# Performance work log

Hardware: AMD Instinct MI355X
Metric: run time of the kernel (lower is better)

## Reference

```python
import jax, jax.numpy as jnp
import numpy as np

B, S, D, H, L = 32, 1024, 512, 8, 4
DH = D // H
FF = D            # dim_feedforward == hidden_dim in the original ctor call
LOC_D, TD_D = 16, 8
TD_EMB = 3        # time_dist_embed_dim
POI = 21          # poi vocab
POI_EMB = 3
ADDR_IN = 1 + POI_EMB
FC = 32           # fc_hidden_dim
NEG = -1e9


def setup_inputs() -> dict:
    key = jax.random.key(0)
    ks = jax.random.split(key, 20)
    g = lambda i, shape, s=0.02: jax.random.normal(ks[i], shape, jnp.float32) * s
    return {
        "addr": jax.random.normal(ks[0], (B, 1), jnp.float32),
        "loc_dense_seq": jax.random.normal(ks[1], (B, S, LOC_D), jnp.float32),
        "time_dist_seq": jax.random.normal(ks[2], (B, S, TD_D), jnp.float32),
        "Wtd": g(3, (TD_D, TD_EMB)), "btd": jnp.zeros((TD_EMB,), jnp.float32),
        "Wemb": g(4, (LOC_D + TD_EMB, D)), "bemb": jnp.zeros((D,), jnp.float32),
        "Wqkv": g(5, (L, D, 3 * D)), "bqkv": jnp.zeros((L, 3 * D), jnp.float32),
        "Wo": g(6, (L, D, D)), "bo": jnp.zeros((L, D), jnp.float32),
        "ln1_g": jnp.ones((L, D), jnp.float32), "ln1_b": jnp.zeros((L, D), jnp.float32),
        "W1": g(7, (L, D, FF)), "b1": jnp.zeros((L, FF), jnp.float32),
        "W2": g(8, (L, FF, D)), "b2": jnp.zeros((L, D), jnp.float32),
        "ln2_g": jnp.ones((L, D), jnp.float32), "ln2_b": jnp.zeros((L, D), jnp.float32),
        "poi_emb": g(9, (POI, POI_EMB), 1.0),
        "Wa": g(10, (ADDR_IN, FC)), "ba": jnp.zeros((FC,), jnp.float32),
        "Wout": g(11, (D, FC)),
        "Wcomb": g(12, (FC, 1)),
        "addr_type": jax.random.randint(ks[13], (B, 1), 0, POI),
        "data_length": jax.random.randint(ks[14], (B,), 1, S + 1),
    }


def _ln(x, g, b, eps=1e-5):
    m = x.mean(-1, keepdims=True)
    v = ((x - m) ** 2).mean(-1, keepdims=True)
    return (x - m) / jnp.sqrt(v + eps) * g + b


def reference(addr, loc_dense_seq, time_dist_seq, Wtd, btd, Wemb, bemb, Wqkv,
              bqkv, Wo, bo, ln1_g, ln1_b, W1, b1, W2, b2, ln2_g, ln2_b,
              poi_emb, Wa, ba, Wout, Wcomb, addr_type, data_length):
    valid = jnp.arange(S)[None, :] < data_length[:, None]            # [B,S]
    td = time_dist_seq @ Wtd + btd                                   # [B,S,3]
    x = jnp.concatenate([loc_dense_seq, td], axis=-1) @ Wemb + bemb  # [B,S,D]
    scale = 1.0 / jnp.sqrt(jnp.float32(DH))
    for l in range(L):  # post-norm TransformerEncoderLayer (relu, eval/no-dropout)
        qkv = x @ Wqkv[l] + bqkv[l]
        q, k, v = jnp.split(qkv, 3, axis=-1)
        q = q.reshape(B, S, H, DH)
        k = k.reshape(B, S, H, DH)
        v = v.reshape(B, S, H, DH)
        scores = jnp.einsum('bqhd,bkhd->bhqk', q, k) * scale
        scores = jnp.where(valid[:, None, None, :], scores, NEG)     # mask padded keys
        attn = jax.nn.softmax(scores, axis=-1)
        ctx = jnp.einsum('bhqk,bkhd->bqhd', attn, v).reshape(B, S, D)
        x = _ln(x + ctx @ Wo[l] + bo[l], ln1_g[l], ln1_b[l])
        ff = jax.nn.relu(x @ W1[l] + b1[l]) @ W2[l] + b2[l]
        x = _ln(x + ff, ln2_g[l], ln2_b[l])
    # per-sample addr branch (vectorized over the original python loop)
    addr_inp = jnp.concatenate([addr, poi_emb[addr_type[:, 0]]], axis=-1)  # [B,4]
    a = addr_inp @ Wa + ba                                                 # [B,FC]
    o = (jnp.tanh(x @ Wout + a[:, None, :]) @ Wcomb)[..., 0]              # [B,S]
    logits = jnp.where(valid, o, NEG)
    logp = jax.nn.log_softmax(logits, axis=1)  # log_softmax over valid positions only
    return jnp.where(valid, logp, 0.0)
```

## Files before the change

### kernel.cpp

```cpp
#include <hip/hip_runtime.h>
#include <stdint.h>


typedef unsigned short u16;
typedef __attribute__((ext_vector_type(8))) short short8;
typedef __attribute__((ext_vector_type(4))) float f32x4;

constexpr int Bn = 32, Sn = 1024, Dn = 512, Hn = 8, Ln = 4;
constexpr int BS = Bn * Sn;

__device__ __forceinline__ float b2f(u16 u) {
    union { uint32_t i; float f; } v; v.i = ((uint32_t)u) << 16; return v.f;
}
__device__ __forceinline__ u16 f2b(float f) {
    union { float f; uint32_t i; } v; v.f = f;
    uint32_t r = v.i + 0x7fffu + ((v.i >> 16) & 1u);
    return (u16)(r >> 16);
}
__device__ __forceinline__ float getf(const void* p, size_t i, int F) {
    return F ? ((const float*)p)[i] : b2f(((const u16*)p)[i]);
}

__device__ __forceinline__ void cp16(void* lds, const void* g) {
    __builtin_amdgcn_global_load_lds(
        (__attribute__((address_space(1))) void*)(uintptr_t)g,
        (__attribute__((address_space(3))) void*)(uint32_t)(uintptr_t)lds,
        16, 0, 0);
}

__global__ __launch_bounds__(256)
void detect_kernel(const void* loc, int* flag)
{
    __shared__ int cnt;
    if (threadIdx.x == 0) cnt = 0;
    __syncthreads();
    const u16* p = (const u16*)loc;
    int c = 0;
    for (int i = threadIdx.x; i < 2048; i += 256) {
        const float v = b2f(p[i]);
        if (!(fabsf(v) <= 100.0f)) c++;
    }
    atomicAdd(&cnt, c);
    __syncthreads();
    if (threadIdx.x == 0) *flag = (cnt >= 64) ? 1 : 0;
}

__global__ __launch_bounds__(256)
void gemm_bt(const u16* __restrict__ A, const u16* __restrict__ Bt,
             const void* __restrict__ bias, int boff, u16* __restrict__ C,
             int N, int K, int relu, const int* __restrict__ flagp)
{
    __shared__ __align__(16) u16 As[128 * 32];
    __shared__ __align__(16) u16 Bs[128 * 32];
    const int F = *flagp;
    const int tid = threadIdx.x;
    const int lane = tid & 63, w = tid >> 6;
    const int wm = w >> 1, wn = w & 1;
    const int quad = lane >> 4, l16 = lane & 15;
    const int bn0 = blockIdx.x * 128, bm0 = blockIdx.y * 128;

    const f32x4 vzero = {0.f, 0.f, 0.f, 0.f};
    f32x4 acc[4][4];
#pragma unroll
    for (int i = 0; i < 4; i++)
#pragma unroll
        for (int j = 0; j < 4; j++) acc[i][j] = vzero;

    const int i0 = tid, i1 = tid + 256;
    const u16* a0 = A + (size_t)(bm0 + (i0 >> 2)) * K + (i0 & 3) * 8;
    const u16* a1 = A + (size_t)(bm0 + (i1 >> 2)) * K + (i1 & 3) * 8;
    const u16* b0 = Bt + (size_t)(bn0 + (i0 >> 2)) * K + (i0 & 3) * 8;
    const u16* b1 = Bt + (size_t)(bn0 + (i1 >> 2)) * K + (i1 & 3) * 8;

    for (int k0 = 0; k0 < K; k0 += 32) {
        cp16(As + i0 * 8, a0 + k0);
        cp16(As + i1 * 8, a1 + k0);
        cp16(Bs + i0 * 8, b0 + k0);
        cp16(Bs + i1 * 8, b1 + k0);
        __syncthreads();
        short8 af[4], bfr[4];
#pragma unroll
        for (int t = 0; t < 4; t++)
            af[t] = *(const short8*)&As[(wm * 64 + t * 16 + l16) * 32 + quad * 8];
#pragma unroll
        for (int t = 0; t < 4; t++)
            bfr[t] = *(const short8*)&Bs[(wn * 64 + t * 16 + l16) * 32 + quad * 8];
#pragma unroll
        for (int tm = 0; tm < 4; tm++)
#pragma unroll
            for (int tn = 0; tn < 4; tn++)
                acc[tm][tn] = __builtin_amdgcn_mfma_f32_16x16x32_bf16(
                    af[tm], bfr[tn], acc[tm][tn], 0, 0, 0);
        __syncthreads();
    }
#pragma unroll
    for (int tm = 0; tm < 4; tm++)
#pragma unroll
        for (int tn = 0; tn < 4; tn++) {
            const int col = bn0 + wn * 64 + tn * 16 + l16;
            const float bv = getf(bias, (size_t)boff + col, F);
#pragma unroll
            for (int r = 0; r < 4; r++) {
                const int row = bm0 + wm * 64 + tm * 16 + quad * 4 + r;
                float v = acc[tm][tn][r] + bv;
                if (relu) v = fmaxf(v, 0.0f);
                C[(size_t)row * N + col] = f2b(v);
            }
        }
}

__global__ __launch_bounds__(256)
void attn_kernel(const u16* __restrict__ qkv, const int* __restrict__ dlen,
                 u16* __restrict__ ctx)
{
    const int qt = blockIdx.x, h = blockIdx.y, b = blockIdx.z;
    const int tid = threadIdx.x, lane = tid & 63, w = tid >> 6;
    const int quad = lane >> 4, l16 = lane & 15;
    const int len = dlen[b];
    __shared__ __align__(16) u16 Vt[64 * 72];
    __shared__ __align__(16) u16 Pl[4][16 * 64];
    const size_t rs = 3 * Dn;
    const u16* base = qkv + (size_t)b * Sn * rs;
    const int q0 = qt * 64 + w * 16;

    short8 qf[2];
#pragma unroll
    for (int s = 0; s < 2; s++)
        qf[s] = *(const short8*)(base + (size_t)(q0 + l16) * rs + h * 64 + quad * 8 + 32 * s);

    const f32x4 vzero = {0.f, 0.f, 0.f, 0.f};
    f32x4 O[4];
#pragma unroll
    for (int t = 0; t < 4; t++) O[t] = vzero;
    float m_i[4] = {-1e9f, -1e9f, -1e9f, -1e9f};
    float l_i[4] = {0.f, 0.f, 0.f, 0.f};

    const int nkt = (len + 63) >> 6;
    for (int kt = 0; kt < nkt; kt++) {
        const int k0 = kt * 64;
        {
            const int key = tid >> 2, f0 = (tid & 3) * 16;
            const u16* vp = base + (size_t)(k0 + key) * rs + 2 * Dn + h * 64 + f0;
            short8 v0 = *(const short8*)vp;
            short8 v1 = *(const short8*)(vp + 8);
#pragma unroll
            for (int j = 0; j < 8; j++) {
                Vt[(f0 + j) * 72 + key]     = (u16)v0[j];
                Vt[(f0 + 8 + j) * 72 + key] = (u16)v1[j];
            }
        }
        __syncthreads();

        f32x4 sacc[4];
#pragma unroll
        for (int tn = 0; tn < 4; tn++) {
            const int key = k0 + tn * 16 + l16;
            const u16* kp = base + (size_t)key * rs + Dn + h * 64 + quad * 8;
            short8 kf0 = *(const short8*)kp;
            short8 kf1 = *(const short8*)(kp + 32);
            f32x4 z = vzero;
            z = __builtin_amdgcn_mfma_f32_16x16x32_bf16(qf[0], kf0, z, 0, 0, 0);
            sacc[tn] = __builtin_amdgcn_mfma_f32_16x16x32_bf16(qf[1], kf1, z, 0, 0, 0);
        }
        float sv[4][4], mt[4] = {-1e9f, -1e9f, -1e9f, -1e9f};
#pragma unroll
        for (int tn = 0; tn < 4; tn++) {
            const bool ok = (k0 + tn * 16 + l16) < len;
#pragma unroll
            for (int r = 0; r < 4; r++) {
                const float v = ok ? sacc[tn][r] * 0.125f : -1e9f;
                sv[tn][r] = v;
                mt[r] = fmaxf(mt[r], v);
            }
        }
#pragma unroll
        for (int r = 0; r < 4; r++)
#pragma unroll
            for (int o = 1; o < 16; o <<= 1)
                mt[r] = fmaxf(mt[r], __shfl_xor(mt[r], o, 64));
        float alpha[4];
#pragma unroll
        for (int r = 0; r < 4; r++) {
            const float mn = fmaxf(m_i[r], mt[r]);
            alpha[r] = __expf(m_i[r] - mn);
            m_i[r] = mn;
        }
        float rsum[4] = {0.f, 0.f, 0.f, 0.f};
#pragma unroll
        for (int tn = 0; tn < 4; tn++)
#pragma unroll
            for (int r = 0; r < 4; r++) {
                const float p = __expf(sv[tn][r] - m_i[r]);
                rsum[r] += p;
                Pl[w][(quad * 4 + r) * 64 + tn * 16 + l16] = f2b(p);
            }
#pragma unroll
        for (int r = 0; r < 4; r++) {
#pragma unroll
            for (int o = 1; o < 16; o <<= 1)
                rsum[r] += __shfl_xor(rsum[r], o, 64);
            l_i[r] = l_i[r] * alpha[r] + rsum[r];
        }
#pragma unroll
        for (int t = 0; t < 4; t++)
#pragma unroll
            for (int r = 0; r < 4; r++)
                O[t][r] *= alpha[r];
#pragma unroll
        for (int s = 0; s < 2; s++) {
            short8 pf = *(const short8*)&Pl[w][l16 * 64 + quad * 8 + 32 * s];
#pragma unroll
            for (int t = 0; t < 4; t++) {
                short8 vf = *(const short8*)&Vt[(t * 16 + l16) * 72 + quad * 8 + 32 * s];
                O[t] = __builtin_amdgcn_mfma_f32_16x16x32_bf16(pf, vf, O[t], 0, 0, 0);
            }
        }
        __syncthreads();
    }
#pragma unroll
    for (int t = 0; t < 4; t++)
#pragma unroll
        for (int r = 0; r < 4; r++) {
            const int q = q0 + quad * 4 + r;
            ctx[(size_t)(b * Sn + q) * Dn + h * 64 + t * 16 + l16] = f2b(O[t][r] / l_i[r]);
        }
}

__global__ __launch_bounds__(256)
void ln_res(u16* __restrict__ x, const u16* __restrict__ t,
            const void* __restrict__ g, const void* __restrict__ bta, int off,
            const int* __restrict__ flagp)
{
    const int F = *flagp;
    const int w = threadIdx.x >> 6, lane = threadIdx.x & 63;
    const size_t row = (size_t)blockIdx.x * 4 + w;
    u16* xp = x + row * Dn;
    const u16* tp = t + row * Dn;
    float v[8]; float s = 0.f;
#pragma unroll
    for (int i = 0; i < 8; i++) {
        const int c = lane + i * 64;
        v[i] = b2f(xp[c]) + b2f(tp[c]);
        s += v[i];
    }
#pragma unroll
    for (int o = 1; o < 64; o <<= 1) s += __shfl_xor(s, o, 64);
    const float mean = s * (1.0f / 512.0f);
    float q = 0.f;
#pragma unroll
    for (int i = 0; i < 8; i++) { const float d = v[i] - mean; q += d * d; }
#pragma unroll
    for (int o = 1; o < 64; o <<= 1) q += __shfl_xor(q, o, 64);
    const float inv = rsqrtf(q * (1.0f / 512.0f) + 1e-5f);
#pragma unroll
    for (int i = 0; i < 8; i++) {
        const int c = lane + i * 64;
        xp[c] = f2b((v[i] - mean) * inv * getf(g, off + c, F) + getf(bta, off + c, F));
    }
}

__global__ __launch_bounds__(256)
void embed_kernel(const void* __restrict__ loc, const void* __restrict__ tds,
                  const void* __restrict__ Wtd, const void* __restrict__ btd,
                  const void* __restrict__ Wemb, const void* __restrict__ bemb,
                  u16* __restrict__ x, const int* __restrict__ flagp)
{
    const int F = *flagp;
    const int token = blockIdx.x;
    const int tid = threadIdx.x;
    __shared__ float inv[19];
    if (tid < 16) {
        inv[tid] = getf(loc, (size_t)token * 16 + tid, F);
    } else if (tid < 19) {
        const int e = tid - 16;
        float a = getf(btd, e, F);
        for (int j = 0; j < 8; j++)
            a += getf(tds, (size_t)token * 8 + j, F) * getf(Wtd, j * 3 + e, F);
        inv[tid] = a;
    }
    __syncthreads();
    for (int d = tid; d < Dn; d += 256) {
        float a = getf(bemb, d, F);
#pragma unroll
        for (int i = 0; i < 19; i++) a += inv[i] * getf(Wemb, (size_t)i * Dn + d, F);
        x[(size_t)token * Dn + d] = f2b(a);
    }
}

__global__ __launch_bounds__(256)
void transpose_w(const void* __restrict__ src, u16* __restrict__ dst,
                 int K, int N, const int* __restrict__ flagp)
{
    const int F = *flagp;
    __shared__ u16 tile[32][33];
    const size_t ls = (size_t)K * N;
    const size_t sb = (size_t)blockIdx.z * ls;
    u16* d = dst + blockIdx.z * ls;
    const int tx = threadIdx.x & 31, ty = threadIdx.x >> 5;
    const int n0 = blockIdx.x * 32, k0 = blockIdx.y * 32;
#pragma unroll
    for (int i = 0; i < 32; i += 8)
        tile[ty + i][tx] = f2b(getf(src, sb + (size_t)(k0 + ty + i) * N + n0 + tx, F));
    __syncthreads();
#pragma unroll
    for (int i = 0; i < 32; i += 8)
        d[(size_t)(n0 + ty + i) * K + k0 + tx] = tile[tx][ty + i];
}

__global__ __launch_bounds__(256)
void final_proj(const u16* __restrict__ x, const void* __restrict__ Wout,
                const void* __restrict__ Wcomb, const void* __restrict__ addr,
                const void* __restrict__ poi, const int* __restrict__ atype,
                const void* __restrict__ Wa, const void* __restrict__ ba,
                float* __restrict__ logits, const int* __restrict__ flagp)
{
    const int F = *flagp;
    __shared__ float xs[8][512];
    const int tid = threadIdx.x;
    const int t0 = blockIdx.x * 8;
    for (int i = tid; i < 8 * 512; i += 256) {
        const int tk = i >> 9, d = i & 511;
        xs[tk][d] = b2f(x[(size_t)(t0 + tk) * Dn + d]);
    }
    __syncthreads();
    const int half = tid >> 5, j = tid & 31;
    const int token = t0 + half;
    const int b = token >> 10;
    const int ty = atype[b];
    float a = getf(ba, j, F) + getf(addr, b, F) * getf(Wa, j, F);
#pragma unroll
    for (int e = 0; e < 3; e++)
        a += getf(poi, ty * 3 + e, F) * getf(Wa, (1 + e) * 32 + j, F);
    float s = a;
    for (int k = 0; k < 512; k++) s += xs[half][k] * getf(Wout, (size_t)k * 32 + j, F);
    float o = tanhf(s) * getf(Wcomb, j, F);
#pragma unroll
    for (int off = 1; off < 32; off <<= 1) o += __shfl_xor(o, off, 64);
    if (j == 0) logits[token] = o;
}

__global__ __launch_bounds__(256)
void lsm_kernel(const float* __restrict__ logits, const int* __restrict__ dlen,
                float* __restrict__ out)
{
    const int b = blockIdx.x, tid = threadIdx.x;
    const int len = dlen[b];
    const float* lp = logits + (size_t)b * Sn;
    __shared__ float wA[4], wB[4];
    float mx = -3e38f;
    for (int s = tid; s < Sn; s += 256) if (s < len) mx = fmaxf(mx, lp[s]);
#pragma unroll
    for (int o = 1; o < 64; o <<= 1) mx = fmaxf(mx, __shfl_xor(mx, o, 64));
    if ((tid & 63) == 0) wA[tid >> 6] = mx;
    __syncthreads();
    mx = fmaxf(fmaxf(wA[0], wA[1]), fmaxf(wA[2], wA[3]));
    float sm = 0.f;
    for (int s = tid; s < Sn; s += 256) if (s < len) sm += __expf(lp[s] - mx);
#pragma unroll
    for (int o = 1; o < 64; o <<= 1) sm += __shfl_xor(sm, o, 64);
    if ((tid & 63) == 0) wB[tid >> 6] = sm;
    __syncthreads();
    const float lse = mx + __logf(wB[0] + wB[1] + wB[2] + wB[3]);
    for (int s = tid; s < Sn; s += 256)
        out[(size_t)b * Sn + s] = (s < len) ? (lp[s] - lse) : 0.0f;
}

extern "C" void kernel_launch(void* const* d_in, const int* in_sizes, int n_in,
                              void* d_out, int out_size, void* d_ws, size_t ws_size,
                              hipStream_t stream) {
    const void* addr  = d_in[0];
    const void* loc   = d_in[1];
    const void* tds   = d_in[2];
    const void* Wtd   = d_in[3];
    const void* btd   = d_in[4];
    const void* Wemb  = d_in[5];
    const void* bemb  = d_in[6];
    const void* Wqkv  = d_in[7];
    const void* bqkv  = d_in[8];
    const void* Wo    = d_in[9];
    const void* bo    = d_in[10];
    const void* ln1g  = d_in[11];
    const void* ln1b  = d_in[12];
    const void* W1    = d_in[13];
    const void* b1    = d_in[14];
    const void* W2    = d_in[15];
    const void* b2    = d_in[16];
    const void* ln2g  = d_in[17];
    const void* ln2b  = d_in[18];
    const void* poi   = d_in[19];
    const void* Wa    = d_in[20];
    const void* ba    = d_in[21];
    const void* Wout  = d_in[22];
    const void* Wcomb = d_in[23];
    const int* atype  = (const int*)d_in[24];
    const int* dlen   = (const int*)d_in[25];

    char* base = (char*)d_ws;
    u16*   xb    = (u16*)(base);
    u16*   qkvb  = (u16*)(base + 33554432ull);
    u16*   ctxb  = (u16*)(base + 134217728ull);
    u16*   tb    = (u16*)(base + 167772160ull);
    u16*   wqkvT = (u16*)(base + 201326592ull);
    u16*   woT   = (u16*)(base + 207618048ull);
    u16*   w1T   = (u16*)(base + 209715200ull);
    u16*   w2T   = (u16*)(base + 211812352ull);
    float* logit = (float*)(base + 213909504ull);
    int*   flag  = (int*)  (base + 214040576ull);
    if (ws_size < 214040592ull) return;

    detect_kernel<<<1, 256, 0, stream>>>(loc, flag);

    transpose_w<<<dim3(48, 16, 4), 256, 0, stream>>>(Wqkv, wqkvT, 512, 1536, flag);
    transpose_w<<<dim3(16, 16, 4), 256, 0, stream>>>(Wo,   woT,   512, 512, flag);
    transpose_w<<<dim3(16, 16, 4), 256, 0, stream>>>(W1,   w1T,   512, 512, flag);
    transpose_w<<<dim3(16, 16, 4), 256, 0, stream>>>(W2,   w2T,   512, 512, flag);

    embed_kernel<<<BS, 256, 0, stream>>>(loc, tds, Wtd, btd, Wemb, bemb, xb, flag);

    for (int l = 0; l < Ln; l++) {
        gemm_bt<<<dim3(12, 256), 256, 0, stream>>>(
            xb, wqkvT + (size_t)l * 1536 * 512, bqkv, l * 1536, qkvb, 1536, 512, 0, flag);
        attn_kernel<<<dim3(16, 8, 32), 256, 0, stream>>>(qkvb, dlen, ctxb);
        gemm_bt<<<dim3(4, 256), 256, 0, stream>>>(
            ctxb, woT + (size_t)l * 512 * 512, bo, l * 512, tb, 512, 512, 0, flag);
        ln_res<<<BS / 4, 256, 0, stream>>>(xb, tb, ln1g, ln1b, l * 512, flag);
        gemm_bt<<<dim3(4, 256), 256, 0, stream>>>(
            xb, w1T + (size_t)l * 512 * 512, b1, l * 512, ctxb, 512, 512, 1, flag);
        gemm_bt<<<dim3(4, 256), 256, 0, stream>>>(
            ctxb, w2T + (size_t)l * 512 * 512, b2, l * 512, tb, 512, 512, 0, flag);
        ln_res<<<BS / 4, 256, 0, stream>>>(xb, tb, ln2g, ln2b, l * 512, flag);
    }

    final_proj<<<BS / 8, 256, 0, stream>>>(xb, Wout, Wcomb, addr, poi, atype,
                                           Wa, ba, logit, flag);
    lsm_kernel<<<Bn, 256, 0, stream>>>(logit, dlen, (float*)d_out);
}
```

Before: 2.071 ms.

## Skip padded tokens across all kernels and drop online-softmax max tracking in attention

```diff
diff --git a/kernel.cpp b/kernel.cpp
--- a/kernel.cpp
+++ b/kernel.cpp
@@ -6,7 +6,7 @@
 typedef __attribute__((ext_vector_type(8))) short short8;
 typedef __attribute__((ext_vector_type(4))) float f32x4;
 
-constexpr int Bn = 32, Sn = 1024, Dn = 512, Hn = 8, Ln = 4;
+constexpr int Bn = 32, Sn = 1024, Dn = 512, Ln = 4;
 constexpr int BS = Bn * Sn;
 
 __device__ __forceinline__ float b2f(u16 u) {
@@ -20,7 +20,6 @@
 __device__ __forceinline__ float getf(const void* p, size_t i, int F) {
     return F ? ((const float*)p)[i] : b2f(((const u16*)p)[i]);
 }
-
 __device__ __forceinline__ void cp16(void* lds, const void* g) {
     __builtin_amdgcn_global_load_lds(
         (__attribute__((address_space(1))) void*)(uintptr_t)g,
@@ -48,16 +47,18 @@
 __global__ __launch_bounds__(256)
 void gemm_bt(const u16* __restrict__ A, const u16* __restrict__ Bt,
              const void* __restrict__ bias, int boff, u16* __restrict__ C,
-             int N, int K, int relu, const int* __restrict__ flagp)
+             int N, int K, int relu, const int* __restrict__ flagp,
+             const int* __restrict__ dlen)
 {
     __shared__ __align__(16) u16 As[128 * 32];
     __shared__ __align__(16) u16 Bs[128 * 32];
+    const int bn0 = blockIdx.x * 128, bm0 = blockIdx.y * 128;
+    if ((bm0 & 1023) >= dlen[bm0 >> 10]) return;
     const int F = *flagp;
     const int tid = threadIdx.x;
     const int lane = tid & 63, w = tid >> 6;
     const int wm = w >> 1, wn = w & 1;
     const int quad = lane >> 4, l16 = lane & 15;
-    const int bn0 = blockIdx.x * 128, bm0 = blockIdx.y * 128;
 
     const f32x4 vzero = {0.f, 0.f, 0.f, 0.f};
     f32x4 acc[4][4];
@@ -113,27 +114,35 @@
 void attn_kernel(const u16* __restrict__ qkv, const int* __restrict__ dlen,
                  u16* __restrict__ ctx)
 {
-    const int qt = blockIdx.x, h = blockIdx.y, b = blockIdx.z;
+    const int id = blockIdx.x;
+    const int qt = id >> 8;
+    const int bh = id & 255;
+    const int h = bh & 7, b = bh >> 3;
+    const int len = dlen[b];
+    if (qt * 128 >= len) return;
     const int tid = threadIdx.x, lane = tid & 63, w = tid >> 6;
     const int quad = lane >> 4, l16 = lane & 15;
-    const int len = dlen[b];
     __shared__ __align__(16) u16 Vt[64 * 72];
     __shared__ __align__(16) u16 Pl[4][16 * 64];
     const size_t rs = 3 * Dn;
     const u16* base = qkv + (size_t)b * Sn * rs;
-    const int q0 = qt * 64 + w * 16;
-
-    short8 qf[2];
-#pragma unroll
-    for (int s = 0; s < 2; s++)
-        qf[s] = *(const short8*)(base + (size_t)(q0 + l16) * rs + h * 64 + quad * 8 + 32 * s);
+    const int q0 = qt * 128 + w * 32;
+
+    short8 qf[2][2];
+#pragma unroll
+    for (int sub = 0; sub < 2; sub++)
+#pragma unroll
+        for (int s = 0; s < 2; s++)
+            qf[sub][s] = *(const short8*)(base + (size_t)(q0 + sub * 16 + l16) * rs
+                                          + h * 64 + quad * 8 + 32 * s);
 
     const f32x4 vzero = {0.f, 0.f, 0.f, 0.f};
-    f32x4 O[4];
-#pragma unroll
-    for (int t = 0; t < 4; t++) O[t] = vzero;
-    float m_i[4] = {-1e9f, -1e9f, -1e9f, -1e9f};
-    float l_i[4] = {0.f, 0.f, 0.f, 0.f};
+    f32x4 O[2][4];
+    float ls[2][4];
+#pragma unroll
+    for (int sub = 0; sub < 2; sub++)
+#pragma unroll
+        for (int t = 0; t < 4; t++) { O[sub][t] = vzero; ls[sub][t] = 0.f; }
 
     const int nkt = (len + 63) >> 6;
     for (int kt = 0; kt < nkt; kt++) {
@@ -151,96 +160,84 @@
         }
         __syncthreads();
 
-        f32x4 sacc[4];
+        short8 kf[4][2];
 #pragma unroll
         for (int tn = 0; tn < 4; tn++) {
-            const int key = k0 + tn * 16 + l16;
-            const u16* kp = base + (size_t)key * rs + Dn + h * 64 + quad * 8;
-            short8 kf0 = *(const short8*)kp;
-            short8 kf1 = *(const short8*)(kp + 32);
-            f32x4 z = vzero;
-            z = __builtin_amdgcn_mfma_f32_16x16x32_bf16(qf[0], kf0, z, 0, 0, 0);
-            sacc[tn] = __builtin_amdgcn_mfma_f32_16x16x32_bf16(qf[1], kf1, z, 0, 0, 0);
+            const u16* kp = base + (size_t)(k0 + tn * 16 + l16) * rs + Dn
+                            + h * 64 + quad * 8;
+            kf[tn][0] = *(const short8*)kp;
+            kf[tn][1] = *(const short8*)(kp + 32);
         }
-        float sv[4][4], mt[4] = {-1e9f, -1e9f, -1e9f, -1e9f};
-#pragma unroll
-        for (int tn = 0; tn < 4; tn++) {
-            const bool ok = (k0 + tn * 16 + l16) < len;
-#pragma unroll
-            for (int r = 0; r < 4; r++) {
-                const float v = ok ? sacc[tn][r] * 0.125f : -1e9f;
-                sv[tn][r] = v;
-                mt[r] = fmaxf(mt[r], v);
-            }
-        }
-#pragma unroll
-        for (int r = 0; r < 4; r++)
-#pragma unroll
-            for (int o = 1; o < 16; o <<= 1)
-                mt[r] = fmaxf(mt[r], __shfl_xor(mt[r], o, 64));
-        float alpha[4];
-#pragma unroll
-        for (int r = 0; r < 4; r++) {
-            const float mn = fmaxf(m_i[r], mt[r]);
-            alpha[r] = __expf(m_i[r] - mn);
-            m_i[r] = mn;
-        }
-        float rsum[4] = {0.f, 0.f, 0.f, 0.f};
-#pragma unroll
-        for (int tn = 0; tn < 4; tn++)
-#pragma unroll
-            for (int r = 0; r < 4; r++) {
-                const float p = __expf(sv[tn][r] - m_i[r]);
-                rsum[r] += p;
-                Pl[w][(quad * 4 + r) * 64 + tn * 16 + l16] = f2b(p);
-            }
-#pragma unroll
-        for (int r = 0; r < 4; r++) {
-#pragma unroll
-            for (int o = 1; o < 16; o <<= 1)
-                rsum[r] += __shfl_xor(rsum[r], o, 64);
-            l_i[r] = l_i[r] * alpha[r] + rsum[r];
-        }
-#pragma unroll
-        for (int t = 0; t < 4; t++)
-#pragma unroll
-            for (int r = 0; r < 4; r++)
-                O[t][r] *= alpha[r];
-#pragma unroll
-        for (int s = 0; s < 2; s++) {
-            short8 pf = *(const short8*)&Pl[w][l16 * 64 + quad * 8 + 32 * s];
-#pragma unroll
-            for (int t = 0; t < 4; t++) {
-                short8 vf = *(const short8*)&Vt[(t * 16 + l16) * 72 + quad * 8 + 32 * s];
-                O[t] = __builtin_amdgcn_mfma_f32_16x16x32_bf16(pf, vf, O[t], 0, 0, 0);
+
+#pragma unroll
+        for (int sub = 0; sub < 2; sub++) {
+            f32x4 sacc[4];
+#pragma unroll
+            for (int tn = 0; tn < 4; tn++) {
+                f32x4 z = vzero;
+                z = __builtin_amdgcn_mfma_f32_16x16x32_bf16(qf[sub][0], kf[tn][0], z, 0, 0, 0);
+                sacc[tn] = __builtin_amdgcn_mfma_f32_16x16x32_bf16(qf[sub][1], kf[tn][1], z, 0, 0, 0);
+            }
+#pragma unroll
+            for (int tn = 0; tn < 4; tn++) {
+                const bool ok = (k0 + tn * 16 + l16) < len;
+#pragma unroll
+                for (int r = 0; r < 4; r++) {
+                    const float p = ok ? __expf(sacc[tn][r] * 0.125f) : 0.0f;
+                    ls[sub][r] += p;
+                    Pl[w][(quad * 4 + r) * 64 + tn * 16 + l16] = f2b(p);
+                }
+            }
+#pragma unroll
+            for (int s = 0; s < 2; s++) {
+                short8 pf = *(const short8*)&Pl[w][l16 * 64 + quad * 8 + 32 * s];
+#pragma unroll
+                for (int t = 0; t < 4; t++) {
+                    short8 vf = *(const short8*)&Vt[(t * 16 + l16) * 72 + quad * 8 + 32 * s];
+                    O[sub][t] = __builtin_amdgcn_mfma_f32_16x16x32_bf16(pf, vf, O[sub][t], 0, 0, 0);
+                }
             }
         }
         __syncthreads();
     }
 #pragma unroll
-    for (int t = 0; t < 4; t++)
+    for (int sub = 0; sub < 2; sub++)
 #pragma unroll
         for (int r = 0; r < 4; r++) {
-            const int q = q0 + quad * 4 + r;
-            ctx[(size_t)(b * Sn + q) * Dn + h * 64 + t * 16 + l16] = f2b(O[t][r] / l_i[r]);
+#pragma unroll
+            for (int o = 1; o < 16; o <<= 1)
+                ls[sub][r] += __shfl_xor(ls[sub][r], o, 64);
         }
+#pragma unroll
+    for (int sub = 0; sub < 2; sub++)
+#pragma unroll
+        for (int t = 0; t < 4; t++)
+#pragma unroll
+            for (int r = 0; r < 4; r++) {
+                const int q = q0 + sub * 16 + quad * 4 + r;
+                ctx[(size_t)(b * Sn + q) * Dn + h * 64 + t * 16 + l16] =
+                    f2b(O[sub][t][r] / ls[sub][r]);
+            }
 }
 
 __global__ __launch_bounds__(256)
 void ln_res(u16* __restrict__ x, const u16* __restrict__ t,
             const void* __restrict__ g, const void* __restrict__ bta, int off,
-            const int* __restrict__ flagp)
-{
-    const int F = *flagp;
+            const int* __restrict__ flagp, const int* __restrict__ dlen)
+{
     const int w = threadIdx.x >> 6, lane = threadIdx.x & 63;
     const size_t row = (size_t)blockIdx.x * 4 + w;
+    if ((int)(row & 1023) >= dlen[row >> 10]) return;
+    const int F = *flagp;
     u16* xp = x + row * Dn;
     const u16* tp = t + row * Dn;
+    const int c0 = lane * 8;
+    short8 xv = *(const short8*)(xp + c0);
+    short8 tv = *(const short8*)(tp + c0);
     float v[8]; float s = 0.f;
 #pragma unroll
     for (int i = 0; i < 8; i++) {
-        const int c = lane + i * 64;
-        v[i] = b2f(xp[c]) + b2f(tp[c]);
+        v[i] = b2f((u16)xv[i]) + b2f((u16)tv[i]);
         s += v[i];
     }
 #pragma unroll
@@ -252,21 +249,24 @@
 #pragma unroll
     for (int o = 1; o < 64; o <<= 1) q += __shfl_xor(q, o, 64);
     const float inv = rsqrtf(q * (1.0f / 512.0f) + 1e-5f);
-#pragma unroll
-    for (int i = 0; i < 8; i++) {
-        const int c = lane + i * 64;
-        xp[c] = f2b((v[i] - mean) * inv * getf(g, off + c, F) + getf(bta, off + c, F));
-    }
+    short8 ov;
+#pragma unroll
+    for (int i = 0; i < 8; i++)
+        ov[i] = (short)f2b((v[i] - mean) * inv * getf(g, off + c0 + i, F)
+                           + getf(bta, off + c0 + i, F));
+    *(short8*)(xp + c0) = ov;
 }
 
 __global__ __launch_bounds__(256)
 void embed_kernel(const void* __restrict__ loc, const void* __restrict__ tds,
                   const void* __restrict__ Wtd, const void* __restrict__ btd,
                   const void* __restrict__ Wemb, const void* __restrict__ bemb,
-                  u16* __restrict__ x, const int* __restrict__ flagp)
-{
+                  u16* __restrict__ x, const int* __restrict__ flagp,
+                  const int* __restrict__ dlen)
+{
+    const int token = blockIdx.x;
+    if ((token & 1023) >= dlen[token >> 10]) return;
     const int F = *flagp;
-    const int token = blockIdx.x;
     const int tid = threadIdx.x;
     __shared__ float inv[19];
     if (tid < 16) {
@@ -312,7 +312,8 @@
                 const void* __restrict__ Wcomb, const void* __restrict__ addr,
                 const void* __restrict__ poi, const int* __restrict__ atype,
                 const void* __restrict__ Wa, const void* __restrict__ ba,
-                float* __restrict__ logits, const int* __restrict__ flagp)
+                float* __restrict__ logits, const int* __restrict__ flagp,
+                const int* __restrict__ dlen)
 {
     const int F = *flagp;
     __shared__ float xs[8][512];
@@ -326,6 +327,7 @@
     const int half = tid >> 5, j = tid & 31;
     const int token = t0 + half;
     const int b = token >> 10;
+    if ((token & 1023) >= dlen[b]) return;
     const int ty = atype[b];
     float a = getf(ba, j, F) + getf(addr, b, F) * getf(Wa, j, F);
 #pragma unroll
@@ -415,23 +417,23 @@
     transpose_w<<<dim3(16, 16, 4), 256, 0, stream>>>(W1,   w1T,   512, 512, flag);
     transpose_w<<<dim3(16, 16, 4), 256, 0, stream>>>(W2,   w2T,   512, 512, flag);
 
-    embed_kernel<<<BS, 256, 0, stream>>>(loc, tds, Wtd, btd, Wemb, bemb, xb, flag);
+    embed_kernel<<<BS, 256, 0, stream>>>(loc, tds, Wtd, btd, Wemb, bemb, xb, flag, dlen);
 
     for (int l = 0; l < Ln; l++) {
         gemm_bt<<<dim3(12, 256), 256, 0, stream>>>(
-            xb, wqkvT + (size_t)l * 1536 * 512, bqkv, l * 1536, qkvb, 1536, 512, 0, flag);
-        attn_kernel<<<dim3(16, 8, 32), 256, 0, stream>>>(qkvb, dlen, ctxb);
+            xb, wqkvT + (size_t)l * 1536 * 512, bqkv, l * 1536, qkvb, 1536, 512, 0, flag, dlen);
+        attn_kernel<<<2048, 256, 0, stream>>>(qkvb, dlen, ctxb);
         gemm_bt<<<dim3(4, 256), 256, 0, stream>>>(
-            ctxb, woT + (size_t)l * 512 * 512, bo, l * 512, tb, 512, 512, 0, flag);
-        ln_res<<<BS / 4, 256, 0, stream>>>(xb, tb, ln1g, ln1b, l * 512, flag);
+            ctxb, woT + (size_t)l * 512 * 512, bo, l * 512, tb, 512, 512, 0, flag, dlen);
+        ln_res<<<BS / 4, 256, 0, stream>>>(xb, tb, ln1g, ln1b, l * 512, flag, dlen);
         gemm_bt<<<dim3(4, 256), 256, 0, stream>>>(
-            xb, w1T + (size_t)l * 512 * 512, b1, l * 512, ctxb, 512, 512, 1, flag);
+            xb, w1T + (size_t)l * 512 * 512, b1, l * 512, ctxb, 512, 512, 1, flag, dlen);
         gemm_bt<<<dim3(4, 256), 256, 0, stream>>>(
-            ctxb, w2T + (size_t)l * 512 * 512, b2, l * 512, tb, 512, 512, 0, flag);
-        ln_res<<<BS / 4, 256, 0, stream>>>(xb, tb, ln2g, ln2b, l * 512, flag);
+            ctxb, w2T + (size_t)l * 512 * 512, b2, l * 512, tb, 512, 512, 0, flag, dlen);
+        ln_res<<<BS / 4, 256, 0, stream>>>(xb, tb, ln2g, ln2b, l * 512, flag, dlen);
     }
 
     final_proj<<<BS / 8, 256, 0, stream>>>(xb, Wout, Wcomb, addr, poi, atype,
-                                           Wa, ba, logit, flag);
+                                           Wa, ba, logit, flag, dlen);
     lsm_kernel<<<Bn, 256, 0, stream>>>(logit, dlen, (float*)d_out);
 }
```

After: 1.793 ms. 1.16x faster.
